# Performance work log

Measured on AMD Instinct MI355X. Metric: run time of the kernel, lower is better.

The kernel has to match this reference:

```python
import jax, jax.numpy as jnp
import numpy as np

N, D_IN = 16384, 1024
E, K = 16, 2
D_EMB, H_UNITS, D_HID = 128, 1024, 512


def setup_inputs() -> dict:
    key = jax.random.key(0)
    ks = jax.random.split(key, 10)
    s = lambda fan_in: 1.0 / np.sqrt(fan_in)
    return {
        "x": jax.random.normal(ks[0], (N, D_IN), jnp.float32),
        "Wr": jax.random.normal(ks[1], (D_IN, D_EMB), jnp.float32) * s(D_IN),
        "br": jnp.zeros((D_EMB,), jnp.float32),
        "expert_embeddings": jax.random.normal(ks[2], (E, D_EMB), jnp.float32) * s(D_EMB),
        "W1": jax.random.normal(ks[3], (E, D_IN, H_UNITS), jnp.float32) * s(D_IN),
        "b1": jnp.zeros((E, H_UNITS), jnp.float32),
        "W2": jax.random.normal(ks[4], (E, H_UNITS, H_UNITS // 2), jnp.float32) * s(H_UNITS),
        "b2": jnp.zeros((E, H_UNITS // 2), jnp.float32),
        "W3": jax.random.normal(ks[5], (E, H_UNITS // 2, D_HID), jnp.float32) * s(H_UNITS // 2),
        "b3": jnp.zeros((E, D_HID), jnp.float32),
    }


def reference(x, Wr, br, expert_embeddings, W1, b1, W2, b2, W3, b3):
    # Router: query per token [N, D_EMB]
    q = x @ Wr + br
    # Negative squared L2 distance to each expert embedding -> scores [N, E]
    d2 = jnp.sum(jnp.square(q[:, None, :] - expert_embeddings[None, :, :]), axis=-1)
    scores = -d2
    # Top-k gating (softmax over the k selected scores only)
    top_k_scores, top_k_idx = jax.lax.top_k(scores, K)        # [N, K]
    gates = jax.nn.softmax(top_k_scores, axis=-1)             # [N, K]
    # Dense all-expert MLP (as the original: every expert on every token)
    h1 = jax.nn.relu(jnp.einsum('nd,edh->enh', x, W1) + b1[:, None, :])   # [E,N,1024]
    h2 = jax.nn.relu(jnp.einsum('enh,ehm->enm', h1, W2) + b2[:, None, :]) # [E,N,512]
    eo = jnp.einsum('enm,emo->eno', h2, W3) + b3[:, None, :]              # [E,N,D_HID]
    eo_t = jnp.transpose(eo, (1, 0, 2))                                   # [N,E,D_HID]
    # Gather top-k expert outputs per token and combine with gates
    sel = jnp.take_along_axis(eo_t, top_k_idx[:, :, None], axis=1)        # [N,K,D_HID]
    combined = jnp.sum(sel * gates[:, :, None], axis=1)                   # [N,D_HID]
    return combined
```

## Files before the change

kernel.cpp:

```cpp
#include <hip/hip_runtime.h>

typedef unsigned short u16;
typedef __attribute__((ext_vector_type(8))) short short8;
typedef __attribute__((ext_vector_type(16))) float f32x16;

#define N_TOK 16384
#define DIN   1024
#define NE    16
#define DEMB  128
#define H1N   1024
#define H2N   512
#define DOUT  512
#define CAP   36864
#define RBLK  1024

#define OFF_P      0ul
#define OFF_C      65536ul
#define OFF_CTRL   65792ul
#define OFF_E01    66048ul
#define OFF_G01    197120ul
#define OFF_GTOK   328192ul
#define OFF_GGATE  475648ul
#define OFF_TSLOT  623104ul
#define OFF_BH     754176ul
#define OFF_BB     819712ul
#define OFF_W2T    885248ul
#define OFF_W3T    17662464ul
#define OFF_W1T    26051072ul
#define OFF_XBF    59605504ul
#define OFF_H1     93159936ul
#define OFF_EO     OFF_H1
#define OFF_H2     OFF_W1T

__device__ __forceinline__ u16 f2bf(float f) {
  union { float f; unsigned u; } v; v.f = f;
  unsigned r = v.u + 0x7fff + ((v.u >> 16) & 1);
  return (u16)(r >> 16);
}

__device__ __forceinline__ void async_copy16(const u16* g, u16* l) {
  __builtin_amdgcn_global_load_lds((const __attribute__((address_space(1))) unsigned*)g,
                                   (__attribute__((address_space(3))) unsigned*)l,
                                   16, 0, 0);
}

__global__ void router_prep(const float* __restrict__ Wr, const float* __restrict__ br,
                            const float* __restrict__ emb, float* __restrict__ P,
                            float* __restrict__ c) {
  int idx = blockIdx.x * 256 + threadIdx.x;
  int row = idx >> 4, e = idx & 15;
  float s = 0.f;
  for (int j = 0; j < DEMB; ++j) s += Wr[row * DEMB + j] * emb[e * DEMB + j];
  P[row * NE + e] = 2.f * s;
  if (idx < NE) {
    float cc = 0.f, n2 = 0.f;
    for (int j = 0; j < DEMB; ++j) {
      float ev = emb[idx * DEMB + j];
      cc += br[j] * ev;
      n2 += ev * ev;
    }
    c[idx] = 2.f * cc - n2;
  }
}

__global__ void __launch_bounds__(256) router_score(
    const float* __restrict__ x, const float* __restrict__ P,
    const float* __restrict__ c, int* __restrict__ e01,
    float* __restrict__ g01, int* __restrict__ bhist,
    u16* __restrict__ xbf) {
  __shared__ float xs[16384];
  __shared__ int lh[16];
  int wave = threadIdx.x >> 6, lane = threadIdx.x & 63;
  int e2 = lane & 7, kgl = lane >> 3;
  int tbase = blockIdx.x * 16 + wave * 4;
  float* xw = xs + wave * 4096;

  if (threadIdx.x < 16) lh[threadIdx.x] = 0;

  u16* xbrow = xbf + (size_t)tbase * DIN;
  #pragma unroll
  for (int t = 0; t < 4; ++t) {
    const float* src = x + (size_t)(tbase + t) * DIN;
    #pragma unroll
    for (int q = 0; q < 4; ++q) {
      int g = q * 256 + lane * 4;
      float4 v = *(const float4*)(src + g);
      *(float4*)(xw + t * 1024 + g) = v;
      ushort4 o;
      o.x = f2bf(v.x); o.y = f2bf(v.y); o.z = f2bf(v.z); o.w = f2bf(v.w);
      *(ushort4*)(xbrow + t * DIN + g) = o;
    }
  }
  __syncthreads();

  int te0 = 2 * e2, te1 = te0 + 1;
  float ce0 = c[te0], ce1 = c[te1];
  const float* Pb = P + te0;

  float acc0[4] = {0.f, 0.f, 0.f, 0.f};
  float acc1[4] = {0.f, 0.f, 0.f, 0.f};
  int cbase = kgl * 128;
  #pragma unroll 4
  for (int i = 0; i < 32; ++i) {
    int w = (kgl * 4 + i * 4) & 127;
    int idx = cbase + w;
    float2 pv0 = *(const float2*)(Pb + (size_t)(idx + 0) * NE);
    float2 pv1 = *(const float2*)(Pb + (size_t)(idx + 1) * NE);
    float2 pv2 = *(const float2*)(Pb + (size_t)(idx + 2) * NE);
    float2 pv3 = *(const float2*)(Pb + (size_t)(idx + 3) * NE);
    #pragma unroll
    for (int t = 0; t < 4; ++t) {
      float4 xv = *(const float4*)(xw + t * 1024 + idx);
      acc0[t] = fmaf(xv.x, pv0.x, acc0[t]); acc1[t] = fmaf(xv.x, pv0.y, acc1[t]);
      acc0[t] = fmaf(xv.y, pv1.x, acc0[t]); acc1[t] = fmaf(xv.y, pv1.y, acc1[t]);
      acc0[t] = fmaf(xv.z, pv2.x, acc0[t]); acc1[t] = fmaf(xv.z, pv2.y, acc1[t]);
      acc0[t] = fmaf(xv.w, pv3.x, acc0[t]); acc1[t] = fmaf(xv.w, pv3.y, acc1[t]);
    }
  }

  for (int t = 0; t < 4; ++t) {
    float s0 = acc0[t], s1 = acc1[t];
    #pragma unroll
    for (int off = 8; off <= 32; off <<= 1) {
      s0 += __shfl_xor(s0, off);
      s1 += __shfl_xor(s1, off);
    }
    s0 += ce0; s1 += ce1;
    float hi; int hidx;
    if (s0 >= s1) { hi = s0; hidx = te0; } else { hi = s1; hidx = te1; }
    float m1 = hi; int i1 = hidx;
    #pragma unroll
    for (int off = 1; off < 8; off <<= 1) {
      float so = __shfl_xor(m1, off); int io = __shfl_xor(i1, off);
      if (so > m1 || (so == m1 && io < i1)) { m1 = so; i1 = io; }
    }
    float c2; int c2i;
    if (i1 == te0)      { c2 = s1; c2i = te1; }
    else if (i1 == te1) { c2 = s0; c2i = te0; }
    else                { c2 = hi; c2i = hidx; }
    float m2 = c2; int i2 = c2i;
    #pragma unroll
    for (int off = 1; off < 8; off <<= 1) {
      float so = __shfl_xor(m2, off); int io = __shfl_xor(i2, off);
      if (so > m2 || (so == m2 && io < i2)) { m2 = so; i2 = io; }
    }
    if (lane == 0) {
      int tok = tbase + t;
      float ev = expf(m2 - m1);
      float inv = 1.f / (1.f + ev);
      e01[tok * 2 + 0] = i1; e01[tok * 2 + 1] = i2;
      g01[tok * 2 + 0] = inv; g01[tok * 2 + 1] = ev * inv;
      atomicAdd(&lh[i1], 1);
      atomicAdd(&lh[i2], 1);
    }
  }
  __syncthreads();
  if (threadIdx.x < 16) bhist[blockIdx.x * 16 + threadIdx.x] = lh[threadIdx.x];
}

__global__ void __launch_bounds__(1024) scan_offsets(
    const int* __restrict__ bhist, int* __restrict__ counts,
    int* __restrict__ poff, int* __restrict__ bbase, int* __restrict__ gtok) {
  int t = threadIdx.x;
  int e = t & 15, ch = t >> 4;
  int b0 = ch * 16;
  int s = 0;
  #pragma unroll
  for (int i = 0; i < 16; ++i) s += bhist[(b0 + i) * 16 + e];
  __shared__ int part[64][16];
  __shared__ int chbase[64][16];
  __shared__ int cnt[16];
  __shared__ int pof[16];
  part[ch][e] = s;
  __syncthreads();
  if (t < 16) {
    int run = 0;
    for (int c2 = 0; c2 < 64; ++c2) { chbase[c2][t] = run; run += part[c2][t]; }
    cnt[t] = run;
  }
  __syncthreads();
  if (t == 0) {
    int off = 0;
    for (int e2 = 0; e2 < NE; ++e2) {
      pof[e2] = off;
      poff[e2] = off;
      counts[e2] = cnt[e2];
      off += (cnt[e2] + 255) & ~255;
    }
    poff[NE] = off;
  }
  __syncthreads();
  int padc = ((cnt[e] + 255) & ~255) - cnt[e];
  int pbase = pof[e] + cnt[e];
  for (int i = ch; i < padc; i += 64) gtok[pbase + i] = 0;

  int run = pof[e] + chbase[ch][e];
  #pragma unroll
  for (int i = 0; i < 16; ++i) {
    bbase[(b0 + i) * 16 + e] = run;
    run += bhist[(b0 + i) * 16 + e];
  }
}

__global__ void build_lists(const int* __restrict__ e01, const float* __restrict__ g01,
                            const int* __restrict__ bbase, int* __restrict__ gtok,
                            float* __restrict__ ggate, int* __restrict__ tslot) {
  __shared__ int pos[16];
  int tid = threadIdx.x;
  if (tid < 16) pos[tid] = bbase[blockIdx.x * 16 + tid];
  __syncthreads();
  if (tid < 16) {
    int t = blockIdx.x * 16 + tid;
    #pragma unroll
    for (int k = 0; k < 2; ++k) {
      int e = e01[t * 2 + k];
      int p = atomicAdd(&pos[e], 1);
      gtok[p] = t;
      ggate[p] = g01[t * 2 + k];
      tslot[t * 2 + k] = p;
    }
  }
}

template<int K, int N>
__global__ void conv_w(const float* __restrict__ W, u16* __restrict__ WT) {
  __shared__ float tile[64][65];
  int e = blockIdx.z;
  int n0 = blockIdx.x * 64, k0 = blockIdx.y * 64;
  int tx = threadIdx.x & 63, ty = threadIdx.x >> 6;
  const float* Wb = W + (size_t)e * K * N;
  #pragma unroll
  for (int p = 0; p < 16; ++p) {
    int k = p * 4 + ty;
    tile[k][tx] = Wb[(size_t)(k0 + k) * N + n0 + tx];
  }
  __syncthreads();
  u16* WTb = WT + (size_t)e * N * K;
  #pragma unroll
  for (int p = 0; p < 16; ++p) {
    int n = p * 4 + ty;
    WTb[(size_t)(n0 + n) * K + k0 + tx] = f2bf(tile[tx][n]);
  }
}

template<int MODE, bool INDIR>
__global__ void __launch_bounds__(256, 2)
gemm_moe(const u16* __restrict__ A, const u16* __restrict__ Ball,
         const float* __restrict__ bias, u16* __restrict__ Cb, float* __restrict__ outF,
         const int* __restrict__ poff, const int* __restrict__ counts,
         const int* __restrict__ gtok, const float* __restrict__ ggate,
         int K, int N, int nblk) {
  __shared__ u16 Asm[3][8192];
  __shared__ u16 Bsm[3][4096];

  int bid = blockIdx.x;
  int q = nblk >> 3, r = nblk & 7;
  int xcd = bid & 7, sidx = bid >> 3;
  int wg = (xcd < r ? xcd * (q + 1) : r * (q + 1) + (xcd - r) * q) + sidx;
  int NB = N >> 7;
  int rb = wg / NB, nb = wg - rb * NB;

  int row_base = rb * 256;
  if (row_base >= poff[NE]) return;
  int e = 0;
  while (row_base >= poff[e + 1]) ++e;

  int tid = threadIdx.x;
  int wave = tid >> 6, lane = tid & 63;
  int wm = wave >> 1, wn = wave & 1;
  int n_base = nb * 128;

  const u16* Brow = Ball + (size_t)e * N * K + (size_t)n_base * K;

  int r0 = tid >> 2;
  int ch8 = ((tid & 3) ^ ((r0 >> 1) & 3)) * 8;
  const u16 *a0, *a1, *a2, *a3;
  if constexpr (INDIR) {
    a0 = A + (size_t)gtok[row_base + r0 +   0] * K;
    a1 = A + (size_t)gtok[row_base + r0 +  64] * K;
    a2 = A + (size_t)gtok[row_base + r0 + 128] * K;
    a3 = A + (size_t)gtok[row_base + r0 + 192] * K;
  } else {
    a0 = A + (size_t)(row_base + r0 +   0) * K;
    a1 = A + (size_t)(row_base + r0 +  64) * K;
    a2 = A + (size_t)(row_base + r0 + 128) * K;
    a3 = A + (size_t)(row_base + r0 + 192) * K;
  }
  const u16* b0 = Brow + (size_t)r0 * K;
  const u16* b1 = Brow + (size_t)(r0 + 64) * K;

  f32x16 acc[4][2];
  #pragma unroll
  for (int m = 0; m < 4; ++m)
    #pragma unroll
    for (int n = 0; n < 2; ++n)
      acc[m][n] = (f32x16)(0.f);

  auto stage_tile = [&](int buf, int kt) {
    async_copy16(a0 + kt + ch8, &Asm[buf][tid * 8]);
    async_copy16(a1 + kt + ch8, &Asm[buf][(256 + tid) * 8]);
    async_copy16(a2 + kt + ch8, &Asm[buf][(512 + tid) * 8]);
    async_copy16(a3 + kt + ch8, &Asm[buf][(768 + tid) * 8]);
    async_copy16(b0 + kt + ch8, &Bsm[buf][tid * 8]);
    async_copy16(b1 + kt + ch8, &Bsm[buf][(256 + tid) * 8]);
  };

  stage_tile(0, 0);
  stage_tile(1, 32);

  int rowA = lane & 31, hm = lane >> 5;
  int swzr = (rowA >> 1) & 3;

  int nstep = K >> 5;
  int rd = 0, st = 2;
  for (int s = 0; s < nstep; ++s) {
    if (s == nstep - 1)
      asm volatile("s_waitcnt vmcnt(0)\n\ts_barrier" ::: "memory");
    else
      asm volatile("s_waitcnt vmcnt(6)\n\ts_barrier" ::: "memory");
    if (s + 2 < nstep) stage_tile(st, (s + 2) << 5);
    short8 av[4][2], bv[2][2];
    #pragma unroll
    for (int m = 0; m < 4; ++m)
      #pragma unroll
      for (int s2 = 0; s2 < 2; ++s2)
        av[m][s2] = *(const short8*)(&Asm[rd][(wm * 128 + m * 32 + rowA) * 32 +
                                             (((s2 << 1) + hm) ^ swzr) * 8]);
    #pragma unroll
    for (int n = 0; n < 2; ++n)
      #pragma unroll
      for (int s2 = 0; s2 < 2; ++s2)
        bv[n][s2] = *(const short8*)(&Bsm[rd][(wn * 64 + n * 32 + rowA) * 32 +
                                             (((s2 << 1) + hm) ^ swzr) * 8]);
    #pragma unroll
    for (int m = 0; m < 4; ++m)
      #pragma unroll
      for (int n = 0; n < 2; ++n)
        #pragma unroll
        for (int s2 = 0; s2 < 2; ++s2)
          acc[m][n] = __builtin_amdgcn_mfma_f32_32x32x16_bf16(av[m][s2], bv[n][s2],
                                                              acc[m][n], 0, 0, 0);
    rd = rd == 2 ? 0 : rd + 1;
    st = st == 2 ? 0 : st + 1;
  }

  int ccol = lane & 31;
  int crow4 = 4 * hm;
  const float* be = bias + (size_t)e * N;
  #pragma unroll
  for (int m = 0; m < 4; ++m) {
    int gr_base = row_base + wm * 128 + m * 32;
    #pragma unroll
    for (int n = 0; n < 2; ++n) {
      int gc = n_base + wn * 64 + n * 32 + ccol;
      float bvs = be[gc];
      #pragma unroll
      for (int reg = 0; reg < 16; ++reg) {
        int rowf = (reg & 3) + 8 * (reg >> 2) + crow4;
        int gr = gr_base + rowf;
        if constexpr (MODE == 0) {
          float v = acc[m][n][reg] + bvs;
          v = v > 0.f ? v : 0.f;
          Cb[(size_t)gr * N + gc] = f2bf(v);
        } else {
          outF[(size_t)gr * N + gc] = acc[m][n][reg] + bvs;
        }
      }
    }
  }
}

__global__ void __launch_bounds__(256) combine_out(
    const float* __restrict__ eo, const int* __restrict__ tslot,
    const float* __restrict__ g01, float* __restrict__ out) {
  int wave = threadIdx.x >> 6, lane = threadIdx.x & 63;
  int tok = blockIdx.x * 4 + wave;
  int s0 = tslot[tok * 2 + 0], s1 = tslot[tok * 2 + 1];
  float g0 = g01[tok * 2 + 0], g1 = g01[tok * 2 + 1];
  const float* r0 = eo + (size_t)s0 * DOUT + lane * 8;
  const float* r1 = eo + (size_t)s1 * DOUT + lane * 8;
  float* o = out + (size_t)tok * DOUT + lane * 8;
  #pragma unroll
  for (int j = 0; j < 2; ++j) {
    float4 v0 = ((const float4*)r0)[j];
    float4 v1 = ((const float4*)r1)[j];
    float4 ov;
    ov.x = g0 * v0.x + g1 * v1.x;
    ov.y = g0 * v0.y + g1 * v1.y;
    ov.z = g0 * v0.z + g1 * v1.z;
    ov.w = g0 * v0.w + g1 * v1.w;
    ((float4*)o)[j] = ov;
  }
}

extern "C" void kernel_launch(void* const* d_in, const int* in_sizes, int n_in,
                              void* d_out, int out_size, void* d_ws, size_t ws_size,
                              hipStream_t stream) {
  const float* x   = (const float*)d_in[0];
  const float* Wr  = (const float*)d_in[1];
  const float* br  = (const float*)d_in[2];
  const float* emb = (const float*)d_in[3];
  const float* W1  = (const float*)d_in[4];
  const float* b1  = (const float*)d_in[5];
  const float* W2  = (const float*)d_in[6];
  const float* b2  = (const float*)d_in[7];
  const float* W3  = (const float*)d_in[8];
  const float* b3  = (const float*)d_in[9];
  float* out = (float*)d_out;
  char* ws = (char*)d_ws;

  float* P      = (float*)(ws + OFF_P);
  float* c      = (float*)(ws + OFF_C);
  int*   counts = (int*)(ws + OFF_CTRL);
  int*   poff   = (int*)(ws + OFF_CTRL + 128);
  int*   e01    = (int*)(ws + OFF_E01);
  float* g01    = (float*)(ws + OFF_G01);
  int*   gtok   = (int*)(ws + OFF_GTOK);
  float* ggate  = (float*)(ws + OFF_GGATE);
  int*   tslot  = (int*)(ws + OFF_TSLOT);
  int*   bhist  = (int*)(ws + OFF_BH);
  int*   bbase  = (int*)(ws + OFF_BB);
  u16*   W1T    = (u16*)(ws + OFF_W1T);
  u16*   W2T    = (u16*)(ws + OFF_W2T);
  u16*   W3T    = (u16*)(ws + OFF_W3T);
  u16*   xbf    = (u16*)(ws + OFF_XBF);
  u16*   h1     = (u16*)(ws + OFF_H1);
  u16*   h2     = (u16*)(ws + OFF_H2);
  float* eo     = (float*)(ws + OFF_EO);

  conv_w<DIN, H1N><<<dim3(H1N / 64, DIN / 64, NE), 256, 0, stream>>>(W1, W1T);
  conv_w<H1N, H2N><<<dim3(H2N / 64, H1N / 64, NE), 256, 0, stream>>>(W2, W2T);
  conv_w<H2N, DOUT><<<dim3(DOUT / 64, H2N / 64, NE), 256, 0, stream>>>(W3, W3T);

  router_prep<<<64, 256, 0, stream>>>(Wr, br, emb, P, c);
  router_score<<<RBLK, 256, 0, stream>>>(x, P, c, e01, g01, bhist, xbf);
  scan_offsets<<<1, 1024, 0, stream>>>(bhist, counts, poff, bbase, gtok);
  build_lists<<<RBLK, 64, 0, stream>>>(e01, g01, bbase, gtok, ggate, tslot);

  int nb1 = (H1N / 128) * (CAP / 256);
  int nb2 = (H2N / 128) * (CAP / 256);
  int nb3 = (DOUT / 128) * (CAP / 256);
  gemm_moe<0, true><<<nb1, 256, 0, stream>>>(xbf, W1T, b1, h1, nullptr,
                                             poff, counts, gtok, nullptr, DIN, H1N, nb1);
  gemm_moe<0, false><<<nb2, 256, 0, stream>>>(h1, W2T, b2, h2, nullptr,
                                              poff, counts, nullptr, nullptr, H1N, H2N, nb2);
  gemm_moe<2, false><<<nb3, 256, 0, stream>>>(h2, W3T, b3, nullptr, eo,
                                              poff, counts, nullptr, nullptr, H2N, DOUT, nb3);
  combine_out<<<N_TOK / 4, 256, 0, stream>>>(eo, tslot, g01, out);
}
```

Before: 336.7 us.

## Rewrite expert GEMM as 256x256 tile, 8-wave kernel with ping-pong quadrant schedule

Replaces the 256x128-tile, 4-wave grouped GEMM with a 256x256-tile, 512-thread kernel. Each wave computes four 64x32 quadrants using 16x16x32 bf16 MFMAs, and LDS staging is interleaved between quadrant phases with s_setprio around the MFMA bursts. The aim is more operand reuse per byte loaded and better overlap of async global-to-LDS copies with matrix math. The cost is 128 KB of LDS per block, one block per CU, many barriers per iteration, and fewer blocks in the grid.

```diff
diff --git a/kernel.cpp b/kernel.cpp
--- a/kernel.cpp
+++ b/kernel.cpp
@@ -2,7 +2,7 @@
 
 typedef unsigned short u16;
 typedef __attribute__((ext_vector_type(8))) short short8;
-typedef __attribute__((ext_vector_type(16))) float f32x16;
+typedef __attribute__((ext_vector_type(4))) float f32x4;
 
 #define N_TOK 16384
 #define DIN   1024
@@ -243,131 +243,146 @@
   }
 }
 
+#define BAR  __builtin_amdgcn_s_barrier()
+#define VW4  asm volatile("s_waitcnt vmcnt(4)" ::: "memory")
+
+#define LOAD_A(BUF, HM) { _Pragma("unroll") for (int m = 0; m < 4; ++m) { \
+    const u16* p_ = &Abuf[BUF][(wm * 128 + (HM) * 64 + m * 16 + fr) * 64]; \
+    av[m][0] = *(const short8*)(p_ + ((kq ^ swz3) << 3)); \
+    av[m][1] = *(const short8*)(p_ + (((4 + kq) ^ swz3) << 3)); } }
+
+#define LOAD_B(BV, BUF, HN) { _Pragma("unroll") for (int n = 0; n < 2; ++n) { \
+    const u16* p_ = &Bbuf[BUF][(wn * 64 + (HN) * 32 + n * 16 + fr) * 64]; \
+    BV[n][0] = *(const short8*)(p_ + ((kq ^ swz3) << 3)); \
+    BV[n][1] = *(const short8*)(p_ + (((4 + kq) ^ swz3) << 3)); } }
+
+#define PH_MFMA(ACC, BV) { __builtin_amdgcn_s_setprio(1); \
+  _Pragma("unroll") for (int m = 0; m < 4; ++m) \
+  _Pragma("unroll") for (int n = 0; n < 2; ++n) { \
+    ACC[m][n] = __builtin_amdgcn_mfma_f32_16x16x32_bf16(av[m][0], BV[n][0], ACC[m][n], 0, 0, 0); \
+    ACC[m][n] = __builtin_amdgcn_mfma_f32_16x16x32_bf16(av[m][1], BV[n][1], ACC[m][n], 0, 0, 0); } \
+  __builtin_amdgcn_s_setprio(0); }
+
+#define EPI(ACC, RO, CO) { _Pragma("unroll") for (int m = 0; m < 4; ++m) { \
+    int gr0 = row_base + wm * 128 + (RO) + m * 16 + crow; \
+    _Pragma("unroll") for (int n = 0; n < 2; ++n) { \
+      int gc = n_base + wn * 64 + (CO) + n * 16 + ccol; \
+      float bvs = be[gc]; \
+      _Pragma("unroll") for (int r2 = 0; r2 < 4; ++r2) { \
+        if constexpr (MODE == 0) { \
+          float v = ACC[m][n][r2] + bvs; v = v > 0.f ? v : 0.f; \
+          Cb[(size_t)(gr0 + r2) * N + gc] = f2bf(v); \
+        } else { \
+          outF[(size_t)(gr0 + r2) * N + gc] = ACC[m][n][r2] + bvs; } } } } }
+
 template<int MODE, bool INDIR>
-__global__ void __launch_bounds__(256, 2)
-gemm_moe(const u16* __restrict__ A, const u16* __restrict__ Ball,
-         const float* __restrict__ bias, u16* __restrict__ Cb, float* __restrict__ outF,
-         const int* __restrict__ poff, const int* __restrict__ counts,
-         const int* __restrict__ gtok, const float* __restrict__ ggate,
-         int K, int N, int nblk) {
-  __shared__ u16 Asm[3][8192];
-  __shared__ u16 Bsm[3][4096];
+__global__ void __launch_bounds__(512)
+gemm_moe256(const u16* __restrict__ A, const u16* __restrict__ Ball,
+            const float* __restrict__ bias, u16* __restrict__ Cb,
+            float* __restrict__ outF, const int* __restrict__ poff,
+            const int* __restrict__ gtok, int K, int N, int nblk) {
+  __shared__ u16 Abuf[2][16384];
+  __shared__ u16 Bbuf[2][16384];
 
   int bid = blockIdx.x;
-  int q = nblk >> 3, r = nblk & 7;
+  int q8 = nblk >> 3, r8 = nblk & 7;
   int xcd = bid & 7, sidx = bid >> 3;
-  int wg = (xcd < r ? xcd * (q + 1) : r * (q + 1) + (xcd - r) * q) + sidx;
-  int NB = N >> 7;
+  int wg = (xcd < r8 ? xcd * (q8 + 1) : r8 * (q8 + 1) + (xcd - r8) * q8) + sidx;
+  int NB = N >> 8;
   int rb = wg / NB, nb = wg - rb * NB;
-
   int row_base = rb * 256;
   if (row_base >= poff[NE]) return;
   int e = 0;
   while (row_base >= poff[e + 1]) ++e;
 
   int tid = threadIdx.x;
-  int wave = tid >> 6, lane = tid & 63;
-  int wm = wave >> 1, wn = wave & 1;
-  int n_base = nb * 128;
-
-  const u16* Brow = Ball + (size_t)e * N * K + (size_t)n_base * K;
-
-  int r0 = tid >> 2;
-  int ch8 = ((tid & 3) ^ ((r0 >> 1) & 3)) * 8;
-  const u16 *a0, *a1, *a2, *a3;
-  if constexpr (INDIR) {
-    a0 = A + (size_t)gtok[row_base + r0 +   0] * K;
-    a1 = A + (size_t)gtok[row_base + r0 +  64] * K;
-    a2 = A + (size_t)gtok[row_base + r0 + 128] * K;
-    a3 = A + (size_t)gtok[row_base + r0 + 192] * K;
-  } else {
-    a0 = A + (size_t)(row_base + r0 +   0) * K;
-    a1 = A + (size_t)(row_base + r0 +  64) * K;
-    a2 = A + (size_t)(row_base + r0 + 128) * K;
-    a3 = A + (size_t)(row_base + r0 + 192) * K;
-  }
-  const u16* b0 = Brow + (size_t)r0 * K;
-  const u16* b1 = Brow + (size_t)(r0 + 64) * K;
-
-  f32x16 acc[4][2];
+  int lane = tid & 63, wv = tid >> 6;
+  int wm = wv >> 2, wn = wv & 3;
+  int fr = lane & 15, kq = lane >> 4;
+  int swz3 = fr & 7;
+  int n_base = nb * 256;
+
+  int l8 = (tid >> 3) & 7;
+  int rbase = ((tid >> 6) << 4) + l8;
+  int csrc = ((tid & 7) ^ l8) << 3;
+
+  const u16 *pA[2][2], *pB[2][2];
+  const u16* Bexp = Ball + (size_t)e * N * K;
+  #pragma unroll
+  for (int h = 0; h < 2; ++h)
+    #pragma unroll
+    for (int j = 0; j < 2; ++j) {
+      int row = h * 128 + rbase + j * 8;
+      if constexpr (INDIR) pA[h][j] = A + (size_t)gtok[row_base + row] * K;
+      else                 pA[h][j] = A + (size_t)(row_base + row) * K;
+      pB[h][j] = Bexp + (size_t)(n_base + row) * K;
+    }
+
+  int ldst = ((tid >> 6) << 10) + ((tid & 63) << 3);
+
+  auto stA = [&](int buf, int h, int kt) {
+    u16* l0 = &Abuf[buf][h * 8192 + ldst];
+    async_copy16(pA[h][0] + kt + csrc, l0);
+    async_copy16(pA[h][1] + kt + csrc, l0 + 512);
+  };
+  auto stB = [&](int buf, int h, int kt) {
+    u16* l0 = &Bbuf[buf][h * 8192 + ldst];
+    async_copy16(pB[h][0] + kt + csrc, l0);
+    async_copy16(pB[h][1] + kt + csrc, l0 + 512);
+  };
+
+  f32x4 q00[4][2], q01[4][2], q11[4][2], q10[4][2];
   #pragma unroll
   for (int m = 0; m < 4; ++m)
     #pragma unroll
-    for (int n = 0; n < 2; ++n)
-      acc[m][n] = (f32x16)(0.f);
-
-  auto stage_tile = [&](int buf, int kt) {
-    async_copy16(a0 + kt + ch8, &Asm[buf][tid * 8]);
-    async_copy16(a1 + kt + ch8, &Asm[buf][(256 + tid) * 8]);
-    async_copy16(a2 + kt + ch8, &Asm[buf][(512 + tid) * 8]);
-    async_copy16(a3 + kt + ch8, &Asm[buf][(768 + tid) * 8]);
-    async_copy16(b0 + kt + ch8, &Bsm[buf][tid * 8]);
-    async_copy16(b1 + kt + ch8, &Bsm[buf][(256 + tid) * 8]);
-  };
-
-  stage_tile(0, 0);
-  stage_tile(1, 32);
-
-  int rowA = lane & 31, hm = lane >> 5;
-  int swzr = (rowA >> 1) & 3;
-
-  int nstep = K >> 5;
-  int rd = 0, st = 2;
-  for (int s = 0; s < nstep; ++s) {
-    if (s == nstep - 1)
-      asm volatile("s_waitcnt vmcnt(0)\n\ts_barrier" ::: "memory");
-    else
-      asm volatile("s_waitcnt vmcnt(6)\n\ts_barrier" ::: "memory");
-    if (s + 2 < nstep) stage_tile(st, (s + 2) << 5);
-    short8 av[4][2], bv[2][2];
-    #pragma unroll
-    for (int m = 0; m < 4; ++m)
-      #pragma unroll
-      for (int s2 = 0; s2 < 2; ++s2)
-        av[m][s2] = *(const short8*)(&Asm[rd][(wm * 128 + m * 32 + rowA) * 32 +
-                                             (((s2 << 1) + hm) ^ swzr) * 8]);
-    #pragma unroll
-    for (int n = 0; n < 2; ++n)
-      #pragma unroll
-      for (int s2 = 0; s2 < 2; ++s2)
-        bv[n][s2] = *(const short8*)(&Bsm[rd][(wn * 64 + n * 32 + rowA) * 32 +
-                                             (((s2 << 1) + hm) ^ swzr) * 8]);
-    #pragma unroll
-    for (int m = 0; m < 4; ++m)
-      #pragma unroll
-      for (int n = 0; n < 2; ++n)
-        #pragma unroll
-        for (int s2 = 0; s2 < 2; ++s2)
-          acc[m][n] = __builtin_amdgcn_mfma_f32_32x32x16_bf16(av[m][s2], bv[n][s2],
-                                                              acc[m][n], 0, 0, 0);
-    rd = rd == 2 ? 0 : rd + 1;
-    st = st == 2 ? 0 : st + 1;
-  }
-
-  int ccol = lane & 31;
-  int crow4 = 4 * hm;
+    for (int n = 0; n < 2; ++n) {
+      q00[m][n] = (f32x4){0.f, 0.f, 0.f, 0.f};
+      q01[m][n] = (f32x4){0.f, 0.f, 0.f, 0.f};
+      q11[m][n] = (f32x4){0.f, 0.f, 0.f, 0.f};
+      q10[m][n] = (f32x4){0.f, 0.f, 0.f, 0.f};
+    }
+  short8 av[4][2], bvlo[2][2], bvhi[2][2];
+
+  stB(0, 0, 0); stB(0, 1, 0); stA(0, 0, 0); stA(0, 1, 0);
+  stB(1, 0, 64); stB(1, 1, 64);
+  VW4;
+  BAR;
+
+  int niter = K >> 7;
+  for (int it = 0; it < niter; ++it) {
+    int kt0 = it << 7;
+    int ktn0 = (it + 1 < niter) ? (kt0 + 128) : kt0;
+    int ktn1 = ktn0 + 64;
+    LOAD_A(0, 0); LOAD_B(bvlo, 0, 0);
+    stA(1, 0, kt0 + 64);
+    BAR; PH_MFMA(q00, bvlo); BAR;
+    LOAD_B(bvhi, 0, 1);
+    stA(1, 1, kt0 + 64);
+    BAR; PH_MFMA(q01, bvhi); BAR;
+    LOAD_A(0, 1);
+    stB(0, 0, ktn0);
+    BAR; PH_MFMA(q11, bvhi); BAR;
+    stB(0, 1, ktn0);
+    VW4;
+    BAR; PH_MFMA(q10, bvlo); BAR;
+    LOAD_A(1, 0); LOAD_B(bvlo, 1, 0);
+    stA(0, 0, ktn0);
+    BAR; PH_MFMA(q00, bvlo); BAR;
+    LOAD_B(bvhi, 1, 1);
+    stA(0, 1, ktn0);
+    BAR; PH_MFMA(q01, bvhi); BAR;
+    LOAD_A(1, 1);
+    stB(1, 0, ktn1);
+    BAR; PH_MFMA(q11, bvhi); BAR;
+    stB(1, 1, ktn1);
+    VW4;
+    BAR; PH_MFMA(q10, bvlo); BAR;
+  }
+
+  int crow = kq * 4;
+  int ccol = fr;
   const float* be = bias + (size_t)e * N;
-  #pragma unroll
-  for (int m = 0; m < 4; ++m) {
-    int gr_base = row_base + wm * 128 + m * 32;
-    #pragma unroll
-    for (int n = 0; n < 2; ++n) {
-      int gc = n_base + wn * 64 + n * 32 + ccol;
-      float bvs = be[gc];
-      #pragma unroll
-      for (int reg = 0; reg < 16; ++reg) {
-        int rowf = (reg & 3) + 8 * (reg >> 2) + crow4;
-        int gr = gr_base + rowf;
-        if constexpr (MODE == 0) {
-          float v = acc[m][n][reg] + bvs;
-          v = v > 0.f ? v : 0.f;
-          Cb[(size_t)gr * N + gc] = f2bf(v);
-        } else {
-          outF[(size_t)gr * N + gc] = acc[m][n][reg] + bvs;
-        }
-      }
-    }
-  }
+  EPI(q00, 0, 0); EPI(q01, 0, 32); EPI(q11, 64, 32); EPI(q10, 64, 0);
 }
 
 __global__ void __launch_bounds__(256) combine_out(
@@ -437,14 +452,14 @@
   scan_offsets<<<1, 1024, 0, stream>>>(bhist, counts, poff, bbase, gtok);
   build_lists<<<RBLK, 64, 0, stream>>>(e01, g01, bbase, gtok, ggate, tslot);
 
-  int nb1 = (H1N / 128) * (CAP / 256);
-  int nb2 = (H2N / 128) * (CAP / 256);
-  int nb3 = (DOUT / 128) * (CAP / 256);
-  gemm_moe<0, true><<<nb1, 256, 0, stream>>>(xbf, W1T, b1, h1, nullptr,
-                                             poff, counts, gtok, nullptr, DIN, H1N, nb1);
-  gemm_moe<0, false><<<nb2, 256, 0, stream>>>(h1, W2T, b2, h2, nullptr,
-                                              poff, counts, nullptr, nullptr, H1N, H2N, nb2);
-  gemm_moe<2, false><<<nb3, 256, 0, stream>>>(h2, W3T, b3, nullptr, eo,
-                                              poff, counts, nullptr, nullptr, H2N, DOUT, nb3);
+  int nb1 = (H1N >> 8) * (CAP / 256);
+  int nb2 = (H2N >> 8) * (CAP / 256);
+  int nb3 = (DOUT >> 8) * (CAP / 256);
+  gemm_moe256<0, true><<<nb1, 512, 0, stream>>>(xbf, W1T, b1, h1, nullptr,
+                                                poff, gtok, DIN, H1N, nb1);
+  gemm_moe256<0, false><<<nb2, 512, 0, stream>>>(h1, W2T, b2, h2, nullptr,
+                                                 poff, nullptr, H1N, H2N, nb2);
+  gemm_moe256<2, false><<<nb3, 512, 0, stream>>>(h2, W3T, b3, nullptr, eo,
+                                                 poff, nullptr, H2N, DOUT, nb3);
   combine_out<<<N_TOK / 4, 256, 0, stream>>>(eo, tslot, g01, out);
 }
```

Result: no change. 330.9 us (-1.7%).
